# Optimization experiments

Hardware: AMD Instinct MI355X
Metric: run time of the kernel (lower is better)

Reference implementation:

```python
import jax, jax.numpy as jnp
import numpy as np
from jax import lax

EPS = 1e-5

def _layernorm(x, g, b):
    m = jnp.mean(x, axis=-1, keepdims=True)
    v = jnp.mean((x - m) ** 2, axis=-1, keepdims=True)
    return (x - m) * lax.rsqrt(v + EPS) * g + b

def _dwconv(x, H, W, w, b):
    # x: [B, N, C], w: [C, 1, 3, 3] (OIHW, depthwise), b: [C]
    B, N, C = x.shape
    xi = x.transpose(0, 2, 1).reshape(B, C, H, W)
    y = lax.conv_general_dilated(
        xi, w, window_strides=(1, 1), padding='SAME',
        feature_group_count=C,
        dimension_numbers=('NCHW', 'OIHW', 'NCHW'))
    y = y + b[None, :, None, None]
    return y.reshape(B, C, H * W).transpose(0, 2, 1)

def _channel_attn(x, groups, qkv_w, qkv_b, proj_w, proj_b):
    B, N, C = x.shape
    hd = C // groups
    qkv = x @ qkv_w.T + qkv_b                       # [B, N, 3C]
    qkv = qkv.reshape(B, N, 3, groups, hd)
    q, k, v = qkv[:, :, 0], qkv[:, :, 1], qkv[:, :, 2]   # [B, N, g, hd]
    q = q * (float(N) ** -0.5)
    attn = jnp.einsum('bngc,bngd->bgcd', q, k)      # [B, g, hd, hd]
    attn = jax.nn.softmax(attn, axis=-1)
    out = jnp.einsum('bgcd,bngd->bngc', attn, v)    # [B, N, g, hd]
    out = out.reshape(B, N, C)
    return out @ proj_w.T + proj_b

def _block(x, H, W, dw1_w, dw1_b, ln1_g, ln1_b, qkv_w, qkv_b, proj_w, proj_b,
           dw2_w, dw2_b, ln2_g, ln2_b, fc1_w, fc1_b, fc2_w, fc2_b, groups=8):
    # conv1 (no norm) + residual
    x = x + _dwconv(x, H, W, dw1_w, dw1_b)
    # prenorm channel attention + residual
    x = x + _channel_attn(_layernorm(x, ln1_g, ln1_b), groups, qkv_w, qkv_b, proj_w, proj_b)
    # conv2 (no norm) + residual
    x = x + _dwconv(x, H, W, dw2_w, dw2_b)
    # prenorm MLP + residual
    h = _layernorm(x, ln2_g, ln2_b)
    h = jax.nn.gelu(h @ fc1_w.T + fc1_b, approximate=False)
    x = x + (h @ fc2_w.T + fc2_b)
    return x

def setup_inputs() -> dict:
    key = jax.random.key(0)
    B, H, W, C, groups, ratio = 32, 32, 32, 768, 8, 4
    N, Ch = H * W, C * ratio
    ks = jax.random.split(key, 16)
    s = lambda fan: 1.0 / np.sqrt(fan)
    return {
        'x': jax.random.normal(ks[0], (B, N, C), jnp.float32),
        'H': H, 'W': W,
        'dw1_w': jax.random.normal(ks[1], (C, 1, 3, 3), jnp.float32) * s(9),
        'dw1_b': jnp.zeros((C,), jnp.float32),
        'ln1_g': jnp.ones((C,), jnp.float32),
        'ln1_b': jnp.zeros((C,), jnp.float32),
        'qkv_w': jax.random.normal(ks[2], (3 * C, C), jnp.float32) * s(C),
        'qkv_b': jnp.zeros((3 * C,), jnp.float32),
        'proj_w': jax.random.normal(ks[3], (C, C), jnp.float32) * s(C),
        'proj_b': jnp.zeros((C,), jnp.float32),
        'dw2_w': jax.random.normal(ks[4], (C, 1, 3, 3), jnp.float32) * s(9),
        'dw2_b': jnp.zeros((C,), jnp.float32),
        'ln2_g': jnp.ones((C,), jnp.float32),
        'ln2_b': jnp.zeros((C,), jnp.float32),
        'fc1_w': jax.random.normal(ks[5], (Ch, C), jnp.float32) * s(C),
        'fc1_b': jnp.zeros((Ch,), jnp.float32),
        'fc2_w': jax.random.normal(ks[6], (C, Ch), jnp.float32) * s(Ch),
        'fc2_b': jnp.zeros((C,), jnp.float32),
    }

def reference(x, H, W, dw1_w, dw1_b, ln1_g, ln1_b, qkv_w, qkv_b, proj_w, proj_b,
              dw2_w, dw2_b, ln2_g, ln2_b, fc1_w, fc1_b, fc2_w, fc2_b):
    return _block(x, H, W, dw1_w, dw1_b, ln1_g, ln1_b, qkv_w, qkv_b, proj_w, proj_b,
                  dw2_w, dw2_b, ln2_g, ln2_b, fc1_w, fc1_b, fc2_w, fc2_b)
```

## Files before the change

kernel.cpp:

```cpp
#include <hip/hip_runtime.h>

typedef unsigned short ushort_t;
typedef __bf16 v8bf __attribute__((ext_vector_type(8)));
typedef float v4f __attribute__((ext_vector_type(4)));

#define B_ 32
#define N_ 1024
#define C_ 768
#define G_ 8
#define HD_ 96
#define CH_ 3072
#define M_ 32768

static __device__ __forceinline__ float b2f(ushort_t u) {
    union { float f; unsigned int i; } z; z.i = ((unsigned int)u) << 16; return z.f;
}
static __device__ __forceinline__ ushort_t f2b(float f) {
    unsigned int u = __float_as_uint(f);
    u += 0x7fff + ((u >> 16) & 1);
    return (ushort_t)(u >> 16);
}
static __device__ __forceinline__ unsigned int pk2(float a, float b) {
    return (unsigned int)f2b(a) | ((unsigned int)f2b(b) << 16);
}

#define GLOAD_LDS16(g, l) __builtin_amdgcn_global_load_lds( \
    (const __attribute__((address_space(1))) unsigned int*)(g), \
    (__attribute__((address_space(3))) unsigned int*)(l), 16, 0, 0)

__global__ __launch_bounds__(256) void cvt_all(
    const float* __restrict__ a, const float* __restrict__ b,
    const float* __restrict__ c, const float* __restrict__ d,
    ushort_t* __restrict__ o)
{
    int blk = blockIdx.x;
    const float* src; ushort_t* dst; int off;
    if (blk < 1728)      { src = a; dst = o;                          off = blk; }
    else if (blk < 2304) { src = b; dst = o + 2304 * 768;             off = blk - 1728; }
    else if (blk < 4608) { src = c; dst = o + 2304 * 768 + 768 * 768; off = blk - 2304; }
    else                 { src = d; dst = o + 2304 * 768 + 768 * 768 + 3072 * 768; off = blk - 4608; }
    int i = (off * 256 + threadIdx.x) * 4;
    float4 v = *(const float4*)(src + i);
    uint2 p; p.x = pk2(v.x, v.y); p.y = pk2(v.z, v.w);
    *(uint2*)(dst + i) = p;
}

__global__ __launch_bounds__(256) void transpose_w2(
    const float* __restrict__ w1, const float* __restrict__ w2,
    float* __restrict__ wt1, float* __restrict__ wt2)
{
    int blk = blockIdx.x;
    const float* w = (blk < 27) ? w1 : w2;
    float* wt = (blk < 27) ? wt1 : wt2;
    int i = (blk % 27) * 256 + threadIdx.x;
    int c = i / 9, k = i % 9;
    wt[k * C_ + c] = w[i];
}

__global__ __launch_bounds__(256) void dwconv_add(
    const float* __restrict__ xin, const float* __restrict__ wt,
    const float* __restrict__ bias, float* __restrict__ out)
{
    int t = threadIdx.x;
    int bid = blockIdx.x;
    int cblk = bid % 6;
    int bhp = bid / 6;
    int b = bhp >> 4, hp = bhp & 15;
    int h0 = hp * 2;
    int tw = t >> 5;
    int c0 = cblk * 128 + (t & 31) * 4;
    int w0 = tw * 4;

    float4 tap[4][6];
#pragma unroll
    for (int dh = 0; dh < 4; dh++) {
        int hh = h0 + dh - 1;
        bool hok = (hh >= 0) && (hh < 32);
#pragma unroll
        for (int dw = 0; dw < 6; dw++) {
            int ww = w0 + dw - 1;
            bool ok = hok && (ww >= 0) && (ww < 32);
            if (ok)
                tap[dh][dw] = *(const float4*)(
                    xin + (size_t)((b << 10) | (hh << 5) | ww) * C_ + c0);
            else
                tap[dh][dw] = make_float4(0.f, 0.f, 0.f, 0.f);
        }
    }
    float4 wv[9];
#pragma unroll
    for (int k = 0; k < 9; k++)
        wv[k] = *(const float4*)(wt + k * C_ + c0);
    float4 bv = *(const float4*)(bias + c0);

#pragma unroll
    for (int row = 0; row < 2; row++) {
#pragma unroll
        for (int i = 0; i < 4; i++) {
            float4 acc = bv;
#pragma unroll
            for (int dh = 0; dh < 3; dh++)
#pragma unroll
                for (int dw = 0; dw < 3; dw++) {
                    float4 xv = tap[row + dh][i + dw];
                    float4 wk = wv[dh * 3 + dw];
                    acc.x += wk.x * xv.x; acc.y += wk.y * xv.y;
                    acc.z += wk.z * xv.z; acc.w += wk.w * xv.w;
                }
            float4 xr = tap[row + 1][i + 1];
            acc.x += xr.x; acc.y += xr.y; acc.z += xr.z; acc.w += xr.w;
            *(float4*)(out + (size_t)((b << 10) | ((h0 + row) << 5) | (w0 + i)) * C_ + c0) = acc;
        }
    }
}

__global__ __launch_bounds__(256) void layernorm_bf(
    const float* __restrict__ xin, const float* __restrict__ g,
    const float* __restrict__ bb, ushort_t* __restrict__ out)
{
    int row = blockIdx.x;
    int t = threadIdx.x;
    const float* xr = xin + (size_t)row * C_;
    float x0 = xr[t], x1 = xr[t + 256], x2 = xr[t + 512];
    float s1 = x0 + x1 + x2;
    float s2 = x0 * x0 + x1 * x1 + x2 * x2;
#pragma unroll
    for (int o = 32; o > 0; o >>= 1) {
        s1 += __shfl_xor(s1, o);
        s2 += __shfl_xor(s2, o);
    }
    __shared__ float red[8];
    if ((t & 63) == 0) { red[(t >> 6) * 2] = s1; red[(t >> 6) * 2 + 1] = s2; }
    __syncthreads();
    s1 = red[0] + red[2] + red[4] + red[6];
    s2 = red[1] + red[3] + red[5] + red[7];
    float m = s1 * (1.0f / 768.0f);
    float var = s2 * (1.0f / 768.0f) - m * m;
    float inv = rsqrtf(var + 1e-5f);
    ushort_t* orow = out + (size_t)row * C_;
    orow[t]       = f2b((x0 - m) * inv * g[t]       + bb[t]);
    orow[t + 256] = f2b((x1 - m) * inv * g[t + 256] + bb[t + 256]);
    orow[t + 512] = f2b((x2 - m) * inv * g[t + 512] + bb[t + 512]);
}

template <int EPI>
__global__ __launch_bounds__(256) void gemm_bt(
    const ushort_t* __restrict__ A, const ushort_t* __restrict__ W,
    const float* __restrict__ bias, const float* __restrict__ resid,
    void* __restrict__ outv, int M, int Nf, int K)
{
    __shared__ __align__(16) ushort_t ring[3][2][4096];
    int t = threadIdx.x;
    int bm = blockIdx.x;
    int bn = blockIdx.y;
    int wave = t >> 6, lane = t & 63;
    int wm = (wave >> 1) * 64;
    int wn = (wave & 1) * 64;
    int row16 = lane & 15;
    int quad = lane >> 4;
    int qswz = (quad * 8) ^ (((row16 >> 1) & 3) * 8);

    int r0 = wave * 16 + (lane >> 2);
    int r1 = (wave + 4) * 16 + (lane >> 2);
    int c8s = ((lane & 3) ^ ((lane >> 3) & 3)) * 8;
    const ushort_t* Ag0 = A + (size_t)(bm * 128 + r0) * K + c8s;
    const ushort_t* Ag1 = A + (size_t)(bm * 128 + r1) * K + c8s;
    const ushort_t* Wg0 = W + (size_t)(bn * 128 + r0) * K + c8s;
    const ushort_t* Wg1 = W + (size_t)(bn * 128 + r1) * K + c8s;

    ushort_t *stA0[3], *stA1[3], *stB0[3], *stB1[3];
    const ushort_t *rdA[3], *rdB[3];
#pragma unroll
    for (int s = 0; s < 3; s++) {
        stA0[s] = &ring[s][0][0] + wave * 512;
        stA1[s] = &ring[s][0][0] + (wave + 4) * 512;
        stB0[s] = &ring[s][1][0] + wave * 512;
        stB1[s] = &ring[s][1][0] + (wave + 4) * 512;
        rdA[s]  = &ring[s][0][0] + (wm + row16) * 32 + qswz;
        rdB[s]  = &ring[s][1][0] + (wn + row16) * 32 + qswz;
    }

    v4f acc[4][4];
#pragma unroll
    for (int i = 0; i < 4; i++)
#pragma unroll
        for (int j = 0; j < 4; j++) acc[i][j] = (v4f){0.f, 0.f, 0.f, 0.f};

    auto STAGE = [&](int s, int off) {
        GLOAD_LDS16(Ag0 + off, stA0[s]);
        GLOAD_LDS16(Ag1 + off, stA1[s]);
        GLOAD_LDS16(Wg0 + off, stB0[s]);
        GLOAD_LDS16(Wg1 + off, stB1[s]);
    };
    auto COMPUTE = [&](int s) {
        v8bf af[4], bfr[4];
#pragma unroll
        for (int i = 0; i < 4; i++) af[i] = *(const v8bf*)(rdA[s] + i * 512);
#pragma unroll
        for (int j = 0; j < 4; j++) bfr[j] = *(const v8bf*)(rdB[s] + j * 512);
        __builtin_amdgcn_s_setprio(1);
#pragma unroll
        for (int i = 0; i < 4; i++)
#pragma unroll
            for (int j = 0; j < 4; j++)
                acc[i][j] = __builtin_amdgcn_mfma_f32_16x16x32_bf16(af[i], bfr[j], acc[i][j], 0, 0, 0);
        __builtin_amdgcn_s_setprio(0);
    };

    STAGE(0, 0);
    STAGE(1, 32);
    asm volatile("s_waitcnt vmcnt(4)" ::: "memory");
    __builtin_amdgcn_s_barrier();

    const int NG = K / 96;
    for (int g = 0; g < NG - 1; ++g) {
        STAGE(2, 64);  COMPUTE(0);
        asm volatile("s_waitcnt vmcnt(4)" ::: "memory");
        __builtin_amdgcn_s_barrier();
        STAGE(0, 96);  COMPUTE(1);
        asm volatile("s_waitcnt vmcnt(4)" ::: "memory");
        __builtin_amdgcn_s_barrier();
        STAGE(1, 128); COMPUTE(2);
        asm volatile("s_waitcnt vmcnt(4)" ::: "memory");
        __builtin_amdgcn_s_barrier();
        Ag0 += 96; Ag1 += 96; Wg0 += 96; Wg1 += 96;
    }
    STAGE(2, 64); COMPUTE(0);
    asm volatile("s_waitcnt vmcnt(4)" ::: "memory");
    __builtin_amdgcn_s_barrier();
    COMPUTE(1);
    asm volatile("s_waitcnt vmcnt(0)" ::: "memory");
    __builtin_amdgcn_s_barrier();
    COMPUTE(2);

    float bv[4];
#pragma unroll
    for (int j = 0; j < 4; j++) bv[j] = bias[bn * 128 + wn + j * 16 + row16];
    int col0 = bn * 128 + wn + row16;
#pragma unroll
    for (int i = 0; i < 4; i++) {
        int rowb = bm * 128 + wm + i * 16 + quad * 4;
#pragma unroll
        for (int r = 0; r < 4; r++) {
            size_t rb = (size_t)(rowb + r) * Nf + col0;
#pragma unroll
            for (int j = 0; j < 4; j++) {
                float v = acc[i][j][r] + bv[j];
                if (EPI == 1) {
                    float u = v * (0.7978845608f + 0.0356774081f * v * v);
                    v = v / (1.0f + __expf(-2.0f * u));
                }
                if (EPI == 2) {
                    v += resid[rb + j * 16];
                    ((float*)outv)[rb + j * 16] = v;
                } else {
                    ((ushort_t*)outv)[rb + j * 16] = f2b(v);
                }
            }
        }
    }
}

__global__ __launch_bounds__(256) void chan_attn(
    const ushort_t* __restrict__ qkv, ushort_t* __restrict__ P)
{
    __shared__ __align__(16) char smem[96 * 97 * 4];
    ushort_t* sQt = (ushort_t*)smem;
    ushort_t* sKt = (ushort_t*)(smem + 13824);
    float* sS = (float*)smem;
    int bg = blockIdx.x;
    int b = bg >> 3, g = bg & 7;
    int t = threadIdx.x;
    int wave = t >> 6, lane = t & 63;
    int wc = (wave >> 1) * 48, wd = (wave & 1) * 48;
    int row16 = lane & 15, quad = lane >> 4;

    int li0 = t * 3;
    int r_[3], sg_[3];
#pragma unroll
    for (int i = 0; i < 3; i++) { r_[i] = (li0 + i) / 12; sg_[i] = (li0 + i) % 12; }

    v4f acc[3][3];
#pragma unroll
    for (int i = 0; i < 3; i++)
#pragma unroll
        for (int j = 0; j < 3; j++) acc[i][j] = (v4f){0.f, 0.f, 0.f, 0.f};

    uint4 uq[3], uk[3];
#pragma unroll
    for (int i = 0; i < 3; i++) {
        const ushort_t* p = qkv + ((size_t)(b * N_ + r_[i]) * 3) * C_ + g * HD_ + sg_[i] * 8;
        uq[i] = *(const uint4*)p;
        uk[i] = *(const uint4*)(p + C_);
    }

    for (int n0 = 0; n0 < N_; n0 += 64) {
        uint4 nq[3] = {}, nk[3] = {};
        bool more = (n0 + 64 < N_);
        if (more) {
#pragma unroll
            for (int i = 0; i < 3; i++) {
                const ushort_t* p = qkv + ((size_t)(b * N_ + n0 + 64 + r_[i]) * 3) * C_ + g * HD_ + sg_[i] * 8;
                nq[i] = *(const uint4*)p;
                nk[i] = *(const uint4*)(p + C_);
            }
        }
        __syncthreads();
#pragma unroll
        for (int i = 0; i < 3; i++) {
            union { uint4 v; ushort_t s[8]; } a, bu;
            a.v = uq[i]; bu.v = uk[i];
#pragma unroll
            for (int k2 = 0; k2 < 8; k2++) {
                sQt[(sg_[i] * 8 + k2) * 72 + r_[i]] = a.s[k2];
                sKt[(sg_[i] * 8 + k2) * 72 + r_[i]] = bu.s[k2];
            }
        }
        __syncthreads();
#pragma unroll
        for (int kk = 0; kk < 64; kk += 32) {
            v8bf af[3], bf2[3];
#pragma unroll
            for (int i = 0; i < 3; i++)
                af[i] = *(const v8bf*)(sQt + (wc + i * 16 + row16) * 72 + kk + quad * 8);
#pragma unroll
            for (int j = 0; j < 3; j++)
                bf2[j] = *(const v8bf*)(sKt + (wd + j * 16 + row16) * 72 + kk + quad * 8);
#pragma unroll
            for (int i = 0; i < 3; i++)
#pragma unroll
                for (int j = 0; j < 3; j++)
                    acc[i][j] = __builtin_amdgcn_mfma_f32_16x16x32_bf16(af[i], bf2[j], acc[i][j], 0, 0, 0);
        }
        if (more) {
#pragma unroll
            for (int i = 0; i < 3; i++) { uq[i] = nq[i]; uk[i] = nk[i]; }
        }
    }
    __syncthreads();
#pragma unroll
    for (int i = 0; i < 3; i++)
#pragma unroll
        for (int j = 0; j < 3; j++)
#pragma unroll
            for (int r = 0; r < 4; r++) {
                int c = wc + i * 16 + quad * 4 + r;
                int d = wd + j * 16 + row16;
                sS[c * 97 + d] = acc[i][j][r] * 0.03125f;
            }
    __syncthreads();
    if (t < 96) {
        float mx = -1e30f;
        for (int d = 0; d < 96; d++) mx = fmaxf(mx, sS[t * 97 + d]);
        float sum = 0.f;
        for (int d = 0; d < 96; d++) sum += __expf(sS[t * 97 + d] - mx);
        float rs = 1.0f / sum;
        ushort_t* prow = P + (size_t)bg * 9216 + t * 96;
        for (int d = 0; d < 96; d++) prow[d] = f2b(__expf(sS[t * 97 + d] - mx) * rs);
    }
}

__global__ __launch_bounds__(256) void attn_av(
    const ushort_t* __restrict__ qkv, const ushort_t* __restrict__ P,
    ushort_t* __restrict__ out)
{
    __shared__ __align__(16) ushort_t sV[256 * 104];
    __shared__ __align__(16) ushort_t sP[96 * 104];
    int blk = blockIdx.x;
    int nch = blk & 3, g = (blk >> 2) & 7, b = blk >> 5;
    int t = threadIdx.x;
    int n0 = nch * 256;
#pragma unroll
    for (int i = 0; i < 12; i++) {
        int li = t + i * 256;
        int r = li / 12, sg = li % 12;
        size_t voff = ((size_t)(b * N_ + n0 + r) * 3 + 2) * C_ + g * HD_ + sg * 8;
        *(uint4*)(sV + r * 104 + sg * 8) = *(const uint4*)(qkv + voff);
    }
#pragma unroll
    for (int i = 0; i < 5; i++) {
        int li = t + i * 256;
        if (li < 1152) {
            int r = li / 12, sg = li % 12;
            *(uint4*)(sP + r * 104 + sg * 8) =
                *(const uint4*)(P + (size_t)(b * 8 + g) * 9216 + li * 8);
        }
    }
    __syncthreads();
    int wave = t >> 6, lane = t & 63;
    int wm = wave * 64;
    int row16 = lane & 15, quad = lane >> 4;
    v4f acc[4][6];
#pragma unroll
    for (int i = 0; i < 4; i++)
#pragma unroll
        for (int j = 0; j < 6; j++) acc[i][j] = (v4f){0.f, 0.f, 0.f, 0.f};
#pragma unroll
    for (int kk = 0; kk < 96; kk += 32) {
        v8bf af[4], bfr[6];
#pragma unroll
        for (int i = 0; i < 4; i++)
            af[i] = *(const v8bf*)(sV + (wm + i * 16 + row16) * 104 + kk + quad * 8);
#pragma unroll
        for (int j = 0; j < 6; j++)
            bfr[j] = *(const v8bf*)(sP + (j * 16 + row16) * 104 + kk + quad * 8);
#pragma unroll
        for (int i = 0; i < 4; i++)
#pragma unroll
            for (int j = 0; j < 6; j++)
                acc[i][j] = __builtin_amdgcn_mfma_f32_16x16x32_bf16(af[i], bfr[j], acc[i][j], 0, 0, 0);
    }
#pragma unroll
    for (int i = 0; i < 4; i++)
#pragma unroll
        for (int j = 0; j < 6; j++)
#pragma unroll
            for (int r = 0; r < 4; r++) {
                int n = n0 + wm + i * 16 + quad * 4 + r;
                int c = j * 16 + row16;
                out[(size_t)(b * N_ + n) * C_ + g * HD_ + c] = f2b(acc[i][j][r]);
            }
}

extern "C" void kernel_launch(void* const* d_in, const int* in_sizes, int n_in,
                              void* d_out, int out_size, void* d_ws, size_t ws_size,
                              hipStream_t stream)
{
    const float* x      = (const float*)d_in[0];
    const float* dw1_w  = (const float*)d_in[3];
    const float* dw1_b  = (const float*)d_in[4];
    const float* ln1_g  = (const float*)d_in[5];
    const float* ln1_b  = (const float*)d_in[6];
    const float* qkv_w  = (const float*)d_in[7];
    const float* qkv_b  = (const float*)d_in[8];
    const float* proj_w = (const float*)d_in[9];
    const float* proj_b = (const float*)d_in[10];
    const float* dw2_w  = (const float*)d_in[11];
    const float* dw2_b  = (const float*)d_in[12];
    const float* ln2_g  = (const float*)d_in[13];
    const float* ln2_b  = (const float*)d_in[14];
    const float* fc1_w  = (const float*)d_in[15];
    const float* fc1_b  = (const float*)d_in[16];
    const float* fc2_w  = (const float*)d_in[17];
    const float* fc2_b  = (const float*)d_in[18];
    float* outp = (float*)d_out;

    char* ws = (char*)d_ws;
    ushort_t* qkvW = (ushort_t*)ws;
    ushort_t* projW = qkvW + 2304 * 768;
    ushort_t* fc1W = projW + 768 * 768;
    ushort_t* fc2W = fc1W + 3072 * 768;
    const size_t WB = (size_t)(2304*768 + 768*768 + 3072*768 + 768*3072) * 2;
    float* wt1 = (float*)(ws + WB);
    float* wt2 = wt1 + 9 * C_;
    const size_t WTB = 2 * 9 * C_ * sizeof(float);

    size_t CB = 32;
    while (CB > 1 && WB + WTB + CB * 12730368ull > ws_size) CB >>= 1;
    const size_t R = CB * 1024;
    char* act = ws + WB + WTB;
    ushort_t* L  = (ushort_t*)act;
    ushort_t* Ab = (ushort_t*)(act + R * C_ * 2);
    float*    X2 = (float*)(act + 2 * R * C_ * 2);
    ushort_t* P  = (ushort_t*)(act + 2 * R * C_ * 2 + R * C_ * 4);
    ushort_t* D  = (ushort_t*)(act + 2 * R * C_ * 2 + R * C_ * 4 + CB * 147456);

    cvt_all<<<6912, 256, 0, stream>>>(qkv_w, proj_w, fc1_w, fc2_w, qkvW);
    transpose_w2<<<54, 256, 0, stream>>>(dw1_w, dw2_w, wt1, wt2);

    dwconv_add<<<32 * 16 * 6, 256, 0, stream>>>(x, wt1, dw1_b, outp);

    const int nchunk = (int)(32 / CB);
    for (int c = 0; c < nchunk; c++) {
        float* xc = outp + (size_t)c * R * C_;
        layernorm_bf<<<(int)R, 256, 0, stream>>>(xc, ln1_g, ln1_b, L);
        gemm_bt<0><<<dim3((int)R / 128, 2304 / 128), 256, 0, stream>>>(
            L, qkvW, qkv_b, nullptr, D, (int)R, 2304, C_);
        chan_attn<<<(int)CB * 8, 256, 0, stream>>>(D, P);
        attn_av<<<(int)CB * 32, 256, 0, stream>>>(D, P, Ab);
        gemm_bt<2><<<dim3((int)R / 128, C_ / 128), 256, 0, stream>>>(
            Ab, projW, proj_b, xc, X2, (int)R, C_, C_);
        dwconv_add<<<(int)(R / 1024) * 16 * 6, 256, 0, stream>>>(X2, wt2, dw2_b, xc);
        layernorm_bf<<<(int)R, 256, 0, stream>>>(xc, ln2_g, ln2_b, L);
        gemm_bt<1><<<dim3((int)R / 128, CH_ / 128), 256, 0, stream>>>(
            L, fc1W, fc1_b, nullptr, D, (int)R, CH_, C_);
        gemm_bt<2><<<dim3((int)R / 128, C_ / 128), 256, 0, stream>>>(
            D, fc2W, fc2_b, xc, xc, (int)R, C_, CH_);
    }
}
```

Before: 1.099 ms.

## Stage dwconv tiles in shared memory and swizzle GEMM block order

The depthwise conv kernel now loads a 6-row by 32-column by 64-channel halo tile into LDS once per block and computes four output rows from it. This replaces per-thread register taps that re-read overlapping neighbours from global memory, cutting redundant global loads at the cost of about 52KB of LDS per block and a barrier. The GEMM also remaps block IDs so eight consecutive blocks share a column of W tiles across adjacent M tiles, aiming for better L2 reuse.

```diff
diff --git a/kernel.cpp b/kernel.cpp
--- a/kernel.cpp
+++ b/kernel.cpp
@@ -61,55 +61,59 @@
     const float* __restrict__ xin, const float* __restrict__ wt,
     const float* __restrict__ bias, float* __restrict__ out)
 {
+    __shared__ float xs[6][32][68];
     int t = threadIdx.x;
     int bid = blockIdx.x;
-    int cblk = bid % 6;
-    int bhp = bid / 6;
-    int b = bhp >> 4, hp = bhp & 15;
-    int h0 = hp * 2;
-    int tw = t >> 5;
-    int c0 = cblk * 128 + (t & 31) * 4;
-    int w0 = tw * 4;
-
-    float4 tap[4][6];
-#pragma unroll
-    for (int dh = 0; dh < 4; dh++) {
-        int hh = h0 + dh - 1;
-        bool hok = (hh >= 0) && (hh < 32);
-#pragma unroll
-        for (int dw = 0; dw < 6; dw++) {
-            int ww = w0 + dw - 1;
-            bool ok = hok && (ww >= 0) && (ww < 32);
-            if (ok)
-                tap[dh][dw] = *(const float4*)(
-                    xin + (size_t)((b << 10) | (hh << 5) | ww) * C_ + c0);
-            else
-                tap[dh][dw] = make_float4(0.f, 0.f, 0.f, 0.f);
-        }
-    }
+    int cb = bid % 12;
+    int bh4 = bid / 12;
+    int b = bh4 >> 3, h4 = bh4 & 7;
+    int h0 = h4 * 4;
+    int c0 = cb * 64;
+    const float* xb = xin + (((size_t)b) << 10) * C_;
+
+#pragma unroll
+    for (int r = 0; r < 6; r++) {
+        int hh = h0 + r - 1;
+        bool ok = (hh >= 0) && (hh < 32);
+#pragma unroll
+        for (int half = 0; half < 2; half++) {
+            int f = t + half * 256;
+            int w = f >> 4, cq = f & 15;
+            float4 v = ok ? *(const float4*)(xb + (size_t)((hh << 5) | w) * C_ + c0 + cq * 4)
+                          : make_float4(0.f, 0.f, 0.f, 0.f);
+            *(float4*)(&xs[r][w][cq * 4]) = v;
+        }
+    }
+    __syncthreads();
+
+    int cq = t & 15, whalf = t >> 4;
     float4 wv[9];
 #pragma unroll
     for (int k = 0; k < 9; k++)
-        wv[k] = *(const float4*)(wt + k * C_ + c0);
-    float4 bv = *(const float4*)(bias + c0);
-
-#pragma unroll
-    for (int row = 0; row < 2; row++) {
-#pragma unroll
-        for (int i = 0; i < 4; i++) {
+        wv[k] = *(const float4*)(wt + k * C_ + c0 + cq * 4);
+    float4 bv = *(const float4*)(bias + c0 + cq * 4);
+
+#pragma unroll
+    for (int hh = 0; hh < 4; hh++) {
+#pragma unroll
+        for (int wi = 0; wi < 2; wi++) {
+            int w = whalf * 2 + wi;
             float4 acc = bv;
 #pragma unroll
             for (int dh = 0; dh < 3; dh++)
 #pragma unroll
                 for (int dw = 0; dw < 3; dw++) {
-                    float4 xv = tap[row + dh][i + dw];
-                    float4 wk = wv[dh * 3 + dw];
-                    acc.x += wk.x * xv.x; acc.y += wk.y * xv.y;
-                    acc.z += wk.z * xv.z; acc.w += wk.w * xv.w;
+                    int ww = w + dw - 1;
+                    if (ww >= 0 && ww < 32) {
+                        float4 xv = *(const float4*)(&xs[hh + dh][ww][cq * 4]);
+                        float4 wk = wv[dh * 3 + dw];
+                        acc.x += wk.x * xv.x; acc.y += wk.y * xv.y;
+                        acc.z += wk.z * xv.z; acc.w += wk.w * xv.w;
+                    }
                 }
-            float4 xr = tap[row + 1][i + 1];
+            float4 xr = *(const float4*)(&xs[hh + 1][w][cq * 4]);
             acc.x += xr.x; acc.y += xr.y; acc.z += xr.z; acc.w += xr.w;
-            *(float4*)(out + (size_t)((b << 10) | ((h0 + row) << 5) | (w0 + i)) * C_ + c0) = acc;
+            *(float4*)(out + (size_t)(((size_t)b << 10) | ((h0 + hh) << 5) | w) * C_ + c0 + cq * 4) = acc;
         }
     }
 }
@@ -151,8 +155,11 @@
 {
     __shared__ __align__(16) ushort_t ring[3][2][4096];
     int t = threadIdx.x;
-    int bm = blockIdx.x;
-    int bn = blockIdx.y;
+    int lid = blockIdx.x + blockIdx.y * gridDim.x;
+    int x8 = lid & 7, P = lid >> 3;
+    int bmc8 = gridDim.x >> 3;
+    int bm = x8 + ((P % bmc8) << 3);
+    int bn = P / bmc8;
     int wave = t >> 6, lane = t & 63;
     int wm = (wave >> 1) * 64;
     int wn = (wave & 1) * 64;
@@ -468,7 +475,7 @@
     cvt_all<<<6912, 256, 0, stream>>>(qkv_w, proj_w, fc1_w, fc2_w, qkvW);
     transpose_w2<<<54, 256, 0, stream>>>(dw1_w, dw2_w, wt1, wt2);
 
-    dwconv_add<<<32 * 16 * 6, 256, 0, stream>>>(x, wt1, dw1_b, outp);
+    dwconv_add<<<32 * 8 * 12, 256, 0, stream>>>(x, wt1, dw1_b, outp);
 
     const int nchunk = (int)(32 / CB);
     for (int c = 0; c < nchunk; c++) {
@@ -480,7 +487,7 @@
         attn_av<<<(int)CB * 32, 256, 0, stream>>>(D, P, Ab);
         gemm_bt<2><<<dim3((int)R / 128, C_ / 128), 256, 0, stream>>>(
             Ab, projW, proj_b, xc, X2, (int)R, C_, C_);
-        dwconv_add<<<(int)(R / 1024) * 16 * 6, 256, 0, stream>>>(X2, wt2, dw2_b, xc);
+        dwconv_add<<<(int)(R / 1024) * 8 * 12, 256, 0, stream>>>(X2, wt2, dw2_b, xc);
         layernorm_bf<<<(int)R, 256, 0, stream>>>(xc, ln2_g, ln2_b, L);
         gemm_bt<1><<<dim3((int)R / 128, CH_ / 128), 256, 0, stream>>>(
             L, fc1W, fc1_b, nullptr, D, (int)R, CH_, C_);
```

New measurement: 1.105 ms. About the same (+0.6%).

## Enlarge GEMM block tile to 256x128 with each wave owning 64x128

Applied to the files above, without the earlier changes.

The bf16 MFMA GEMM block tile grows from 128x128 to 256x128. Each of the four waves now computes a 64x128 sub-tile (4x8 MFMA accumulators) instead of 64x64. The LDS ring stages 256 A rows and 128 W rows per k-step, with six global-to-LDS loads per thread and matching vmcnt waits. The grid M dimension is halved for all four GEMM launches. This raises MFMA work per LDS fragment load and per W byte fetched, at the cost of doubled accumulator registers, more shared memory and fewer blocks, which may reduce occupancy and wave parallelism.

```diff
diff --git a/kernel.cpp b/kernel.cpp
--- a/kernel.cpp
+++ b/kernel.cpp
@@ -149,102 +149,99 @@
     const float* __restrict__ bias, const float* __restrict__ resid,
     void* __restrict__ outv, int M, int Nf, int K)
 {
-    __shared__ __align__(16) ushort_t ring[3][2][4096];
+    __shared__ __align__(16) ushort_t ring[3][12288];
     int t = threadIdx.x;
     int bm = blockIdx.x;
     int bn = blockIdx.y;
     int wave = t >> 6, lane = t & 63;
-    int wm = (wave >> 1) * 64;
-    int wn = (wave & 1) * 64;
+    int wm = wave * 64;
     int row16 = lane & 15;
     int quad = lane >> 4;
     int qswz = (quad * 8) ^ (((row16 >> 1) & 3) * 8);
 
-    int r0 = wave * 16 + (lane >> 2);
-    int r1 = (wave + 4) * 16 + (lane >> 2);
+    int rloc = lane >> 2;
     int c8s = ((lane & 3) ^ ((lane >> 3) & 3)) * 8;
-    const ushort_t* Ag0 = A + (size_t)(bm * 128 + r0) * K + c8s;
-    const ushort_t* Ag1 = A + (size_t)(bm * 128 + r1) * K + c8s;
-    const ushort_t* Wg0 = W + (size_t)(bn * 128 + r0) * K + c8s;
-    const ushort_t* Wg1 = W + (size_t)(bn * 128 + r1) * K + c8s;
-
-    ushort_t *stA0[3], *stA1[3], *stB0[3], *stB1[3];
+    const ushort_t* Ag = A + (size_t)(bm * 256 + wave * 16 + rloc) * K + c8s;
+    const ushort_t* Wg = W + (size_t)(bn * 128 + wave * 16 + rloc) * K + c8s;
+    const size_t a64 = (size_t)64 * K;
+
+    ushort_t *stA[3], *stB[3];
     const ushort_t *rdA[3], *rdB[3];
 #pragma unroll
     for (int s = 0; s < 3; s++) {
-        stA0[s] = &ring[s][0][0] + wave * 512;
-        stA1[s] = &ring[s][0][0] + (wave + 4) * 512;
-        stB0[s] = &ring[s][1][0] + wave * 512;
-        stB1[s] = &ring[s][1][0] + (wave + 4) * 512;
-        rdA[s]  = &ring[s][0][0] + (wm + row16) * 32 + qswz;
-        rdB[s]  = &ring[s][1][0] + (wn + row16) * 32 + qswz;
-    }
-
-    v4f acc[4][4];
+        stA[s] = &ring[s][0] + wave * 512;
+        stB[s] = &ring[s][8192] + wave * 512;
+        rdA[s] = &ring[s][0] + (wm + row16) * 32 + qswz;
+        rdB[s] = &ring[s][8192] + row16 * 32 + qswz;
+    }
+
+    v4f acc[4][8];
 #pragma unroll
     for (int i = 0; i < 4; i++)
 #pragma unroll
-        for (int j = 0; j < 4; j++) acc[i][j] = (v4f){0.f, 0.f, 0.f, 0.f};
+        for (int j = 0; j < 8; j++) acc[i][j] = (v4f){0.f, 0.f, 0.f, 0.f};
 
     auto STAGE = [&](int s, int off) {
-        GLOAD_LDS16(Ag0 + off, stA0[s]);
-        GLOAD_LDS16(Ag1 + off, stA1[s]);
-        GLOAD_LDS16(Wg0 + off, stB0[s]);
-        GLOAD_LDS16(Wg1 + off, stB1[s]);
+        GLOAD_LDS16(Ag + off,           stA[s]);
+        GLOAD_LDS16(Ag + off + a64,     stA[s] + 4 * 512);
+        GLOAD_LDS16(Ag + off + 2 * a64, stA[s] + 8 * 512);
+        GLOAD_LDS16(Ag + off + 3 * a64, stA[s] + 12 * 512);
+        GLOAD_LDS16(Wg + off,           stB[s]);
+        GLOAD_LDS16(Wg + off + a64,     stB[s] + 4 * 512);
     };
     auto COMPUTE = [&](int s) {
-        v8bf af[4], bfr[4];
+        v8bf af[4], bfr[8];
 #pragma unroll
         for (int i = 0; i < 4; i++) af[i] = *(const v8bf*)(rdA[s] + i * 512);
 #pragma unroll
-        for (int j = 0; j < 4; j++) bfr[j] = *(const v8bf*)(rdB[s] + j * 512);
+        for (int j = 0; j < 8; j++) bfr[j] = *(const v8bf*)(rdB[s] + j * 512);
         __builtin_amdgcn_s_setprio(1);
 #pragma unroll
         for (int i = 0; i < 4; i++)
 #pragma unroll
-            for (int j = 0; j < 4; j++)
+            for (int j = 0; j < 8; j++)
                 acc[i][j] = __builtin_amdgcn_mfma_f32_16x16x32_bf16(af[i], bfr[j], acc[i][j], 0, 0, 0);
         __builtin_amdgcn_s_setprio(0);
     };
 
     STAGE(0, 0);
     STAGE(1, 32);
-    asm volatile("s_waitcnt vmcnt(4)" ::: "memory");
+    asm volatile("s_waitcnt vmcnt(6)" ::: "memory");
     __builtin_amdgcn_s_barrier();
 
     const int NG = K / 96;
     for (int g = 0; g < NG - 1; ++g) {
         STAGE(2, 64);  COMPUTE(0);
-        asm volatile("s_waitcnt vmcnt(4)" ::: "memory");
+        asm volatile("s_waitcnt vmcnt(6)" ::: "memory");
         __builtin_amdgcn_s_barrier();
         STAGE(0, 96);  COMPUTE(1);
-        asm volatile("s_waitcnt vmcnt(4)" ::: "memory");
+        asm volatile("s_waitcnt vmcnt(6)" ::: "memory");
         __builtin_amdgcn_s_barrier();
         STAGE(1, 128); COMPUTE(2);
-        asm volatile("s_waitcnt vmcnt(4)" ::: "memory");
+        asm volatile("s_waitcnt vmcnt(6)" ::: "memory");
         __builtin_amdgcn_s_barrier();
-        Ag0 += 96; Ag1 += 96; Wg0 += 96; Wg1 += 96;
+        Ag += 96; Wg += 96;
     }
     STAGE(2, 64); COMPUTE(0);
-    asm volatile("s_waitcnt vmcnt(4)" ::: "memory");
+    asm volatile("s_waitcnt vmcnt(6)" ::: "memory");
     __builtin_amdgcn_s_barrier();
     COMPUTE(1);
     asm volatile("s_waitcnt vmcnt(0)" ::: "memory");
     __builtin_amdgcn_s_barrier();
     COMPUTE(2);
 
-    float bv[4];
-#pragma unroll
-    for (int j = 0; j < 4; j++) bv[j] = bias[bn * 128 + wn + j * 16 + row16];
-    int col0 = bn * 128 + wn + row16;
+    float bv[8];
+#pragma unroll
+    for (int j = 0; j < 8; j++) bv[j] = bias[bn * 128 + j * 16 + row16];
+    int col0 = bn * 128 + row16;
 #pragma unroll
     for (int i = 0; i < 4; i++) {
-        int rowb = bm * 128 + wm + i * 16 + quad * 4;
+        int rowb = bm * 256 + wm + i * 16 + quad * 4;
 #pragma unroll
         for (int r = 0; r < 4; r++) {
             size_t rb = (size_t)(rowb + r) * Nf + col0;
 #pragma unroll
-            for (int j = 0; j < 4; j++) {
+            for (int j = 0; j < 8; j++) {
                 float v = acc[i][j][r] + bv[j];
                 if (EPI == 1) {
                     float u = v * (0.7978845608f + 0.0356774081f * v * v);
@@ -474,17 +471,17 @@
     for (int c = 0; c < nchunk; c++) {
         float* xc = outp + (size_t)c * R * C_;
         layernorm_bf<<<(int)R, 256, 0, stream>>>(xc, ln1_g, ln1_b, L);
-        gemm_bt<0><<<dim3((int)R / 128, 2304 / 128), 256, 0, stream>>>(
+        gemm_bt<0><<<dim3((int)R / 256, 2304 / 128), 256, 0, stream>>>(
             L, qkvW, qkv_b, nullptr, D, (int)R, 2304, C_);
         chan_attn<<<(int)CB * 8, 256, 0, stream>>>(D, P);
         attn_av<<<(int)CB * 32, 256, 0, stream>>>(D, P, Ab);
-        gemm_bt<2><<<dim3((int)R / 128, C_ / 128), 256, 0, stream>>>(
+        gemm_bt<2><<<dim3((int)R / 256, C_ / 128), 256, 0, stream>>>(
             Ab, projW, proj_b, xc, X2, (int)R, C_, C_);
         dwconv_add<<<(int)(R / 1024) * 16 * 6, 256, 0, stream>>>(X2, wt2, dw2_b, xc);
         layernorm_bf<<<(int)R, 256, 0, stream>>>(xc, ln2_g, ln2_b, L);
-        gemm_bt<1><<<dim3((int)R / 128, CH_ / 128), 256, 0, stream>>>(
+        gemm_bt<1><<<dim3((int)R / 256, CH_ / 128), 256, 0, stream>>>(
             L, fc1W, fc1_b, nullptr, D, (int)R, CH_, C_);
-        gemm_bt<2><<<dim3((int)R / 128, C_ / 128), 256, 0, stream>>>(
+        gemm_bt<2><<<dim3((int)R / 256, C_ / 128), 256, 0, stream>>>(
             D, fc2W, fc2_b, xc, xc, (int)R, C_, CH_);
     }
 }
```

Measured after the change: 1.274 ms. +15.9%, slower.
